# Kernel tuning notes

Hardware: AMD Instinct MI355X
Metric: run time of the kernel (lower is better)

## Reference

```python
import jax, jax.numpy as jnp
import numpy as np

DIM = 512
B, S = 4, 2048


def _linear_params(key, d_in, d_out):
    kw, kb = jax.random.split(key)
    bound = 1.0 / np.sqrt(d_in)
    W = jax.random.uniform(kw, (d_out, d_in), minval=-bound, maxval=bound, dtype=jnp.float32)
    b = jax.random.uniform(kb, (d_out,), minval=-bound, maxval=bound, dtype=jnp.float32)
    return W, b


def setup_inputs() -> dict:
    key = jax.random.key(0)
    ks = jax.random.split(key, 6)
    x = jax.random.normal(ks[0], (B, S, DIM), dtype=jnp.float32)
    Wq, bq = _linear_params(ks[1], DIM, DIM)
    Wk, bk = _linear_params(ks[2], DIM, DIM)
    Wv, bv = _linear_params(ks[3], DIM, DIM)
    W1, b1 = _linear_params(ks[4], DIM, 4 * DIM)
    W2, b2 = _linear_params(ks[5], 4 * DIM, DIM)
    return {"x": x, "Wq": Wq, "bq": bq, "Wk": Wk, "bk": bk,
            "Wv": Wv, "bv": bv, "W1": W1, "b1": b1, "W2": W2, "b2": b2}


def reference(x, Wq, bq, Wk, bk, Wv, bv, W1, b1, W2, b2):
    # q, k, v projections (torch Linear: x @ W.T + b)
    q = x @ Wq.T + bq          # [B, S, D]
    k = x @ Wk.T + bk
    v = x @ Wv.T + bv
    # unscaled attention, exactly as in the source (no 1/sqrt(d))
    scores = jnp.einsum('bsd,btd->bst', q, k)   # [B, S, S]
    attn = jax.nn.softmax(scores, axis=-1) @ v  # [B, S, D]
    # 2-layer FFN with ReLU
    h = jax.nn.relu(attn @ W1.T + b1)           # [B, S, 4D]
    return h @ W2.T + b2                        # [B, S, D]
```

## Files before the change

### kernel.cpp

```cpp
#include <hip/hip_runtime.h>
#include <hip/hip_bf16.h>

typedef _Float16  f16x8  __attribute__((ext_vector_type(8)));
typedef float     f32x4  __attribute__((ext_vector_type(4)));
typedef unsigned short u16;
typedef u16       u16x4  __attribute__((ext_vector_type(4)));
typedef u16       u16x8  __attribute__((ext_vector_type(8)));

#define LOG2E 1.44269504f

__device__ __forceinline__ u16 f2h_bits(float f) {
    union { _Float16 h; u16 u; } v; v.h = (_Float16)f; return v.u;
}
__device__ __forceinline__ float h2f(u16 b) {
    union { u16 u; _Float16 h; } v; v.u = b; return (float)v.h;
}

__global__ __launch_bounds__(256)
void cvt_all(const float* __restrict__ x,
             const float* __restrict__ Wq, const float* __restrict__ Wk,
             const float* __restrict__ Wv, const float* __restrict__ W1,
             const float* __restrict__ W2, const float* __restrict__ bq,
             const float* __restrict__ bk, const float* __restrict__ bv,
             u16* __restrict__ x16, u16* __restrict__ Wqkv16,
             u16* __restrict__ W116, u16* __restrict__ W216, float* __restrict__ bqkv) {
    const int i = blockIdx.x * 256 + threadIdx.x;
    constexpr int X4 = 8192 * 512 / 4;
    constexpr int S = 512 * 512 / 4, L = 2048 * 512 / 4;
    const float* src; u16* dst; int j;
    if      (i < X4)                 { src = x;  dst = x16;            j = i;                  }
    else if (i < X4 + S)             { src = Wq; dst = Wqkv16;         j = i - X4;             }
    else if (i < X4 + 2 * S)         { src = Wk; dst = Wqkv16 + 4 * S; j = i - X4 - S;         }
    else if (i < X4 + 3 * S)         { src = Wv; dst = Wqkv16 + 8 * S; j = i - X4 - 2 * S;     }
    else if (i < X4 + 3 * S + L)     { src = W1; dst = W116;           j = i - X4 - 3 * S;     }
    else if (i < X4 + 3 * S + 2 * L) { src = W2; dst = W216;           j = i - X4 - 3 * S - L; }
    else if (i < X4 + 3 * S + 2 * L + 384) {
        const int g = (i - X4 - 3 * S - 2 * L) * 4;
#pragma unroll
        for (int t = 0; t < 4; ++t) {
            const int e = g + t;
            bqkv[e] = (e < 512) ? bq[e] : (e < 1024 ? bk[e - 512] : bv[e - 1024]);
        }
        return;
    } else return;
    f32x4 v = ((const f32x4*)src)[j];
    u16x4 h;
#pragma unroll
    for (int t = 0; t < 4; ++t) h[t] = f2h_bits(v[t]);
    ((u16x4*)dst)[j] = h;
}

template<int ROWS>
__device__ __forceinline__ void stage_rows(const u16* __restrict__ g0, int ld, u16* lds, int wl) {
    const int l = threadIdx.x & 63;
    constexpr int CH = ROWS / 64;
#pragma unroll
    for (int i = 0; i < CH; ++i) {
        const int base = (wl * CH + i) << 10;
        const int off  = base + (l << 4);
        const int row  = off >> 6;
        const int cb   = off & 63;
        const u16* g = g0 + (size_t)row * ld + (cb >> 1);
        __builtin_amdgcn_global_load_lds((const __attribute__((address_space(1))) void*)g,
                                         (__attribute__((address_space(3))) void*)((char*)lds + base),
                                         16, 0, 0);
    }
}

template<int BN, int SPLITK, bool RELU, int OMODE, bool AEXP, typename TC>
__global__ __launch_bounds__(256 * SPLITK, 4)
void gemm16(const u16* __restrict__ Ag, const u16* __restrict__ Bg,
            const float* __restrict__ bias, TC* __restrict__ C,
            void* __restrict__ xtra, const void* __restrict__ xtra2,
            int K, int lda, int ldb, int ldc,
            long sA, long sB, long sC)
{
    const int nx = gridDim.x, ny = gridDim.y;
    const int nwg = nx * ny * gridDim.z;
    int bid = blockIdx.x + nx * (blockIdx.y + ny * blockIdx.z);
    int swz = (bid & 7) * (nwg >> 3) + (bid >> 3);
    const int n0 = (swz % nx) * BN; swz /= nx;
    const int m0 = (swz % ny) * 128;
    const int bz = swz / ny;

    constexpr int FR = (BN == 128) ? 4 : 2;
    constexpr int ATILE = 128 * 32;
    constexpr int BTILE = BN * 32;
    constexpr int BUFSZ = ATILE + BTILE;
    __shared__ __align__(16) u16 smem[SPLITK * 2 * BUFSZ];

    const int l  = threadIdx.x & 63, w = threadIdx.x >> 6;
    const int kw = (SPLITK == 2) ? (w >> 2) : 0;
    const int wl = w & 3;
    const int wr = (BN == 128) ? (wl >> 1) * 64 : wl * 32;
    const int wc = (BN == 128) ? (wl & 1) * 64 : 0;
    const int lr = l & 15, kg = l >> 4;

    const int Kh = K / SPLITK;
    const int kb = kw * Kh;

    const u16* Ab = Ag + (size_t)bz * sA + (size_t)m0 * lda + kb;
    const u16* Bb = Bg + (size_t)bz * sB + (size_t)n0 * ldb + kb;
    const float* Cb = AEXP ? ((const float*)xtra2 + (size_t)bz * 2048 * 32 + (size_t)m0 * 32)
                           : nullptr;
    C += (size_t)bz * sC;

    u16* mybuf = smem + kw * 2 * BUFSZ;

    u16x8 areg0, areg1; float acof0, acof1;
    auto stage_issue = [&](int buf, int k0) {
        u16* s = mybuf + buf * BUFSZ;
        if constexpr (AEXP) {
            {
                const int off = ((wl * 2 + 0) << 10) + (l << 4);
                const int row = off >> 6, col = (off & 63) >> 1;
                areg0 = *(const u16x8*)&Ab[(size_t)row * lda + k0 + col];
                acof0 = Cb[row * 32 + ((kb + k0) >> 6)];
            }
            {
                const int off = ((wl * 2 + 1) << 10) + (l << 4);
                const int row = off >> 6, col = (off & 63) >> 1;
                areg1 = *(const u16x8*)&Ab[(size_t)row * lda + k0 + col];
                acof1 = Cb[row * 32 + ((kb + k0) >> 6)];
            }
        } else {
            stage_rows<128>(Ab + k0, lda, s, wl);
        }
        stage_rows<BN>(Bb + k0, ldb, s + ATILE, wl);
    };
    auto stage_finish = [&](int buf) {
        if constexpr (AEXP) {
            u16* s = mybuf + buf * BUFSZ;
            {
                const int off = ((wl * 2 + 0) << 10) + (l << 4);
                u16x8 o;
#pragma unroll
                for (int j = 0; j < 8; ++j)
                    o[j] = f2h_bits(exp2f(h2f(areg0[j]) * LOG2E + acof0));
                *(u16x8*)((char*)s + off) = o;
            }
            {
                const int off = ((wl * 2 + 1) << 10) + (l << 4);
                u16x8 o;
#pragma unroll
                for (int j = 0; j < 8; ++j)
                    o[j] = f2h_bits(exp2f(h2f(areg1[j]) * LOG2E + acof1));
                *(u16x8*)((char*)s + off) = o;
            }
        }
    };

    f32x4 acc[FR][4] = {};
    auto compute = [&](int buf) {
        const u16* sA = mybuf + buf * BUFSZ;
        const u16* sB = sA + ATILE;
        f16x8 a[FR], b[4];
#pragma unroll
        for (int i = 0; i < FR; ++i) a[i] = *(const f16x8*)&sA[(wr + i * 16 + lr) * 32 + kg * 8];
#pragma unroll
        for (int i = 0; i < 4; ++i)  b[i] = *(const f16x8*)&sB[(wc + i * 16 + lr) * 32 + kg * 8];
#pragma unroll
        for (int mi = 0; mi < FR; ++mi)
#pragma unroll
            for (int ni = 0; ni < 4; ++ni)
                acc[mi][ni] = __builtin_amdgcn_mfma_f32_16x16x32_f16(a[mi], b[ni], acc[mi][ni], 0, 0, 0);
    };

    stage_issue(0, 0);
    stage_finish(0);
    __syncthreads();
    int cur = 0;
    for (int k0 = 0; k0 < Kh; k0 += 32) {
        const bool more = (k0 + 32 < Kh);
        if (more) stage_issue(cur ^ 1, k0 + 32);
        compute(cur);
        if (more) stage_finish(cur ^ 1);
        __syncthreads();
        cur ^= 1;
    }

    if constexpr (SPLITK == 2) {
        float* red = (float*)smem;
        const int slot = (wl * 64 + l) * (FR * 4);
        if (kw == 1) {
#pragma unroll
            for (int mi = 0; mi < FR; ++mi)
#pragma unroll
                for (int ni = 0; ni < 4; ++ni)
                    *(f32x4*)&red[(slot + mi * 4 + ni) * 4] = acc[mi][ni];
        }
        __syncthreads();
        if (kw == 1) return;
#pragma unroll
        for (int mi = 0; mi < FR; ++mi)
#pragma unroll
            for (int ni = 0; ni < 4; ++ni)
                acc[mi][ni] += *(const f32x4*)&red[(slot + mi * 4 + ni) * 4];
    }

    if constexpr (OMODE == 5) {
        float* MB = (float*)xtra + (size_t)bz * 2048 * 32;
        float* SB = (float*)const_cast<void*>(xtra2);
        SB += (size_t)bz * 2048 * 32;
        const int cb = (n0 + wc) >> 6;
#pragma unroll
        for (int mi = 0; mi < FR; ++mi) {
            const int mbase = m0 + wr + mi * 16 + kg * 4;
#pragma unroll
            for (int j = 0; j < 4; ++j) {
                float rmax = fmaxf(fmaxf(acc[mi][0][j], acc[mi][1][j]),
                                   fmaxf(acc[mi][2][j], acc[mi][3][j]));
                rmax = fmaxf(rmax, __shfl_xor(rmax, 1));
                rmax = fmaxf(rmax, __shfl_xor(rmax, 2));
                rmax = fmaxf(rmax, __shfl_xor(rmax, 4));
                rmax = fmaxf(rmax, __shfl_xor(rmax, 8));
                float lsum = 0.0f;
#pragma unroll
                for (int ni = 0; ni < 4; ++ni) lsum += __expf(acc[mi][ni][j] - rmax);
                lsum += __shfl_xor(lsum, 1);
                lsum += __shfl_xor(lsum, 2);
                lsum += __shfl_xor(lsum, 4);
                lsum += __shfl_xor(lsum, 8);
                const int row = mbase + j;
                if (lr == 0) {
                    MB[(size_t)row * 32 + cb] = rmax;
                    SB[(size_t)row * 32 + cb] = lsum;
                }
#pragma unroll
                for (int ni = 0; ni < 4; ++ni)
                    ((u16*)C)[(size_t)row * ldc + (n0 + wc + ni * 16 + lr)] =
                        f2h_bits(acc[mi][ni][j] - rmax);
            }
        }
        return;
    }

#pragma unroll
    for (int mi = 0; mi < FR; ++mi) {
        const int mbase = m0 + wr + mi * 16 + kg * 4;
#pragma unroll
        for (int ni = 0; ni < 4; ++ni) {
            const int n = n0 + wc + ni * 16 + lr;
            const float bv = bias ? bias[n] : 0.0f;
            if constexpr (OMODE == 4) {
                if (n0 < 1024) {
#pragma unroll
                    for (int j = 0; j < 4; ++j)
                        ((u16*)C)[(size_t)(mbase + j) * ldc + n] = f2h_bits(acc[mi][ni][j] + bv);
                } else {
                    const int d  = n - 1024;
                    const int bb = mbase >> 11;
                    const int s  = mbase & 2047;
                    u16x4 o;
#pragma unroll
                    for (int j = 0; j < 4; ++j) o[j] = f2h_bits(acc[mi][ni][j] + bv);
                    *(u16x4*)((u16*)xtra + ((size_t)bb * 512 + d) * 2048 + s) = o;
                }
            } else {
#pragma unroll
                for (int j = 0; j < 4; ++j) {
                    float x = acc[mi][ni][j] + bv;
                    if constexpr (RELU) x = fmaxf(x, 0.0f);
                    const size_t idx = (size_t)(mbase + j) * ldc + n;
                    if constexpr (OMODE == 0) C[idx] = x;
                    else                      ((u16*)C)[idx] = f2h_bits(x);
                }
            }
        }
    }
}

__global__ __launch_bounds__(256)
void softmax_stats(const float* __restrict__ MB, const float* __restrict__ SB,
                   float* __restrict__ Cc) {
    const int row = blockIdx.x * 256 + threadIdx.x;
    const f32x4* mbp = (const f32x4*)(MB + (size_t)row * 32);
    const f32x4* sbp = (const f32x4*)(SB + (size_t)row * 32);
    f32x4 mv[8], sv[8];
#pragma unroll
    for (int i = 0; i < 8; ++i) { mv[i] = mbp[i]; sv[i] = sbp[i]; }
    float m = mv[0][0];
#pragma unroll
    for (int i = 0; i < 8; ++i)
#pragma unroll
        for (int j = 0; j < 4; ++j) m = fmaxf(m, mv[i][j]);
    float s = 0.0f;
#pragma unroll
    for (int i = 0; i < 8; ++i)
#pragma unroll
        for (int j = 0; j < 4; ++j) s += sv[i][j] * __expf(mv[i][j] - m);
    const float lg = __log2f(s);
    f32x4* cp = (f32x4*)(Cc + (size_t)row * 32);
#pragma unroll
    for (int i = 0; i < 8; ++i) {
        f32x4 o;
#pragma unroll
        for (int j = 0; j < 4; ++j) o[j] = (mv[i][j] - m) * LOG2E - lg;
        cp[i] = o;
    }
}

extern "C" void kernel_launch(void* const* d_in, const int* in_sizes, int n_in,
                              void* d_out, int out_size, void* d_ws, size_t ws_size,
                              hipStream_t stream) {
    const float* x  = (const float*)d_in[0];
    const float* Wq = (const float*)d_in[1];
    const float* bq = (const float*)d_in[2];
    const float* Wk = (const float*)d_in[3];
    const float* bk = (const float*)d_in[4];
    const float* Wv = (const float*)d_in[5];
    const float* bv = (const float*)d_in[6];
    const float* W1 = (const float*)d_in[7];
    const float* b1 = (const float*)d_in[8];
    const float* W2 = (const float*)d_in[9];
    const float* b2 = (const float*)d_in[10];
    float* out = (float*)d_out;

    char* ws = (char*)d_ws;
    size_t off = 0;
    auto alloc = [&](size_t bytes) { void* p = ws + off; off += (bytes + 255) & ~(size_t)255; return p; };
    u16* x16    = (u16*)alloc(8192ull * 512 * 2);
    u16* Wqkv16 = (u16*)alloc(1536ull * 512 * 2);
    u16* W116   = (u16*)alloc(2048ull * 512 * 2);
    u16* W216   = (u16*)alloc(512ull * 2048 * 2);
    float* bqkv = (float*)alloc(1536 * 4);
    u16* qk     = (u16*)alloc(8192ull * 1024 * 2);
    u16* s16    = (u16*)alloc(4ull * 2048 * 2048 * 2);
    u16* vt     = (u16*)alloc(4ull * 512 * 2048 * 2);
    float* mb   = (float*)alloc(8192ull * 32 * 4);
    float* sb   = (float*)alloc(8192ull * 32 * 4);
    float* cf   = (float*)alloc(8192ull * 32 * 4);
    u16* attn = x16;
    u16* h    = s16;
    if (ws_size < off) return;

    dim3 blk(256), blk2(512);

    cvt_all<<<dim3(6914), blk, 0, stream>>>(x, Wq, Wk, Wv, W1, W2, bq, bk, bv,
                                            x16, Wqkv16, W116, W216, bqkv);

    gemm16<128, 1, false, 4, false, u16><<<dim3(12, 64, 1), blk, 0, stream>>>(
        x16, Wqkv16, bqkv, qk, vt, nullptr, 512, 512, 512, 1024, 0, 0, 0);
    gemm16<128, 1, false, 5, false, u16><<<dim3(16, 16, 4), blk, 0, stream>>>(
        qk, qk + 512, nullptr, s16, mb, sb, 512, 1024, 1024, 2048,
        2048L * 1024, 2048L * 1024, 2048L * 2048);
    softmax_stats<<<dim3(32), blk, 0, stream>>>(mb, sb, cf);
    gemm16<64, 2, false, 2, true, u16><<<dim3(8, 16, 4), blk2, 0, stream>>>(
        s16, vt, nullptr, attn, nullptr, cf, 2048, 2048, 2048, 512,
        2048L * 2048, 512L * 2048, 2048L * 512);
    gemm16<128, 1, true, 2, false, u16><<<dim3(16, 64, 1), blk, 0, stream>>>(
        attn, W116, b1, h, nullptr, nullptr, 512, 512, 512, 2048, 0, 0, 0);
    gemm16<64, 2, false, 0, false, float><<<dim3(8, 64, 1), blk2, 0, stream>>>(
        h, W216, b2, out, nullptr, nullptr, 2048, 2048, 2048, 512, 0, 0, 0);
}
```

Measured before the change: 199.4 us.

## Store block-local softmax probabilities and rescale PV partials per column block

The QK^T kernel now writes exp(s - local block max) as fp16 instead of the raw shifted scores. The PV GEMM loads A through the async global-to-LDS path instead of doing exp in registers, keeping per-64-column partial accumulators and folding them into the output with a per-row scale factor computed by softmax_stats. This removes the per-element exp from the PV GEMM's A-staging path, at the cost of extra accumulator registers and a scaled accumulate every two k-steps.

Result: faster. 183.1 us (-8.2%).

```diff
diff --git a/kernel.cpp b/kernel.cpp
--- a/kernel.cpp
+++ b/kernel.cpp
@@ -7,13 +7,8 @@
 typedef u16       u16x4  __attribute__((ext_vector_type(4)));
 typedef u16       u16x8  __attribute__((ext_vector_type(8)));
 
-#define LOG2E 1.44269504f
-
 __device__ __forceinline__ u16 f2h_bits(float f) {
     union { _Float16 h; u16 u; } v; v.h = (_Float16)f; return v.u;
-}
-__device__ __forceinline__ float h2f(u16 b) {
-    union { u16 u; _Float16 h; } v; v.u = b; return (float)v.h;
 }
 
 __global__ __launch_bounds__(256)
@@ -67,7 +62,7 @@
     }
 }
 
-template<int BN, int SPLITK, bool RELU, int OMODE, bool AEXP, typename TC>
+template<int BN, int SPLITK, bool RELU, int OMODE, bool PVS, typename TC>
 __global__ __launch_bounds__(256 * SPLITK, 4)
 void gemm16(const u16* __restrict__ Ag, const u16* __restrict__ Bg,
             const float* __restrict__ bias, TC* __restrict__ C,
@@ -101,56 +96,19 @@
 
     const u16* Ab = Ag + (size_t)bz * sA + (size_t)m0 * lda + kb;
     const u16* Bb = Bg + (size_t)bz * sB + (size_t)n0 * ldb + kb;
-    const float* Cb = AEXP ? ((const float*)xtra2 + (size_t)bz * 2048 * 32 + (size_t)m0 * 32)
-                           : nullptr;
+    const float* Cb = PVS ? ((const float*)xtra2 + (size_t)bz * 2048 * 32) : nullptr;
     C += (size_t)bz * sC;
 
     u16* mybuf = smem + kw * 2 * BUFSZ;
 
-    u16x8 areg0, areg1; float acof0, acof1;
-    auto stage_issue = [&](int buf, int k0) {
+    auto stage = [&](int buf, int k0) {
         u16* s = mybuf + buf * BUFSZ;
-        if constexpr (AEXP) {
-            {
-                const int off = ((wl * 2 + 0) << 10) + (l << 4);
-                const int row = off >> 6, col = (off & 63) >> 1;
-                areg0 = *(const u16x8*)&Ab[(size_t)row * lda + k0 + col];
-                acof0 = Cb[row * 32 + ((kb + k0) >> 6)];
-            }
-            {
-                const int off = ((wl * 2 + 1) << 10) + (l << 4);
-                const int row = off >> 6, col = (off & 63) >> 1;
-                areg1 = *(const u16x8*)&Ab[(size_t)row * lda + k0 + col];
-                acof1 = Cb[row * 32 + ((kb + k0) >> 6)];
-            }
-        } else {
-            stage_rows<128>(Ab + k0, lda, s, wl);
-        }
+        stage_rows<128>(Ab + k0, lda, s, wl);
         stage_rows<BN>(Bb + k0, ldb, s + ATILE, wl);
     };
-    auto stage_finish = [&](int buf) {
-        if constexpr (AEXP) {
-            u16* s = mybuf + buf * BUFSZ;
-            {
-                const int off = ((wl * 2 + 0) << 10) + (l << 4);
-                u16x8 o;
-#pragma unroll
-                for (int j = 0; j < 8; ++j)
-                    o[j] = f2h_bits(exp2f(h2f(areg0[j]) * LOG2E + acof0));
-                *(u16x8*)((char*)s + off) = o;
-            }
-            {
-                const int off = ((wl * 2 + 1) << 10) + (l << 4);
-                u16x8 o;
-#pragma unroll
-                for (int j = 0; j < 8; ++j)
-                    o[j] = f2h_bits(exp2f(h2f(areg1[j]) * LOG2E + acof1));
-                *(u16x8*)((char*)s + off) = o;
-            }
-        }
-    };
 
     f32x4 acc[FR][4] = {};
+    f32x4 tmp[FR][4] = {};
     auto compute = [&](int buf) {
         const u16* sA = mybuf + buf * BUFSZ;
         const u16* sB = sA + ATILE;
@@ -162,19 +120,38 @@
 #pragma unroll
         for (int mi = 0; mi < FR; ++mi)
 #pragma unroll
-            for (int ni = 0; ni < 4; ++ni)
-                acc[mi][ni] = __builtin_amdgcn_mfma_f32_16x16x32_f16(a[mi], b[ni], acc[mi][ni], 0, 0, 0);
+            for (int ni = 0; ni < 4; ++ni) {
+                if constexpr (PVS)
+                    tmp[mi][ni] = __builtin_amdgcn_mfma_f32_16x16x32_f16(a[mi], b[ni], tmp[mi][ni], 0, 0, 0);
+                else
+                    acc[mi][ni] = __builtin_amdgcn_mfma_f32_16x16x32_f16(a[mi], b[ni], acc[mi][ni], 0, 0, 0);
+            }
     };
 
-    stage_issue(0, 0);
-    stage_finish(0);
+    stage(0, 0);
     __syncthreads();
     int cur = 0;
     for (int k0 = 0; k0 < Kh; k0 += 32) {
-        const bool more = (k0 + 32 < Kh);
-        if (more) stage_issue(cur ^ 1, k0 + 32);
+        if (k0 + 32 < Kh) stage(cur ^ 1, k0 + 32);
         compute(cur);
-        if (more) stage_finish(cur ^ 1);
+        if constexpr (PVS) {
+            if (k0 & 32) {
+                const int cb = (kb + k0) >> 6;
+#pragma unroll
+                for (int mi = 0; mi < FR; ++mi) {
+                    const int mrow = m0 + wr + mi * 16 + kg * 4;
+                    f32x4 cf4;
+#pragma unroll
+                    for (int j = 0; j < 4; ++j) cf4[j] = Cb[(size_t)(mrow + j) * 32 + cb];
+#pragma unroll
+                    for (int ni = 0; ni < 4; ++ni) {
+#pragma unroll
+                        for (int j = 0; j < 4; ++j) acc[mi][ni][j] += cf4[j] * tmp[mi][ni][j];
+                        tmp[mi][ni] = f32x4{0.f, 0.f, 0.f, 0.f};
+                    }
+                }
+            }
+        }
         __syncthreads();
         cur ^= 1;
     }
@@ -214,9 +191,9 @@
                 rmax = fmaxf(rmax, __shfl_xor(rmax, 2));
                 rmax = fmaxf(rmax, __shfl_xor(rmax, 4));
                 rmax = fmaxf(rmax, __shfl_xor(rmax, 8));
-                float lsum = 0.0f;
-#pragma unroll
-                for (int ni = 0; ni < 4; ++ni) lsum += __expf(acc[mi][ni][j] - rmax);
+                float p[4]; float lsum = 0.0f;
+#pragma unroll
+                for (int ni = 0; ni < 4; ++ni) { p[ni] = __expf(acc[mi][ni][j] - rmax); lsum += p[ni]; }
                 lsum += __shfl_xor(lsum, 1);
                 lsum += __shfl_xor(lsum, 2);
                 lsum += __shfl_xor(lsum, 4);
@@ -228,8 +205,7 @@
                 }
 #pragma unroll
                 for (int ni = 0; ni < 4; ++ni)
-                    ((u16*)C)[(size_t)row * ldc + (n0 + wc + ni * 16 + lr)] =
-                        f2h_bits(acc[mi][ni][j] - rmax);
+                    ((u16*)C)[(size_t)row * ldc + (n0 + wc + ni * 16 + lr)] = f2h_bits(p[ni]);
             }
         }
         return;
@@ -272,7 +248,7 @@
 
 __global__ __launch_bounds__(256)
 void softmax_stats(const float* __restrict__ MB, const float* __restrict__ SB,
-                   float* __restrict__ Cc) {
+                   float* __restrict__ Cf) {
     const int row = blockIdx.x * 256 + threadIdx.x;
     const f32x4* mbp = (const f32x4*)(MB + (size_t)row * 32);
     const f32x4* sbp = (const f32x4*)(SB + (size_t)row * 32);
@@ -284,18 +260,18 @@
     for (int i = 0; i < 8; ++i)
 #pragma unroll
         for (int j = 0; j < 4; ++j) m = fmaxf(m, mv[i][j]);
-    float s = 0.0f;
+    float e[8][4]; float s = 0.0f;
 #pragma unroll
     for (int i = 0; i < 8; ++i)
 #pragma unroll
-        for (int j = 0; j < 4; ++j) s += sv[i][j] * __expf(mv[i][j] - m);
-    const float lg = __log2f(s);
-    f32x4* cp = (f32x4*)(Cc + (size_t)row * 32);
+        for (int j = 0; j < 4; ++j) { e[i][j] = __expf(mv[i][j] - m); s += sv[i][j] * e[i][j]; }
+    const float inv = 1.0f / s;
+    f32x4* cp = (f32x4*)(Cf + (size_t)row * 32);
 #pragma unroll
     for (int i = 0; i < 8; ++i) {
         f32x4 o;
 #pragma unroll
-        for (int j = 0; j < 4; ++j) o[j] = (mv[i][j] - m) * LOG2E - lg;
+        for (int j = 0; j < 4; ++j) o[j] = e[i][j] * inv;
         cp[i] = o;
     }
 }
@@ -325,13 +301,13 @@
     u16* W216   = (u16*)alloc(512ull * 2048 * 2);
     float* bqkv = (float*)alloc(1536 * 4);
     u16* qk     = (u16*)alloc(8192ull * 1024 * 2);
-    u16* s16    = (u16*)alloc(4ull * 2048 * 2048 * 2);
+    u16* p16    = (u16*)alloc(4ull * 2048 * 2048 * 2);
     u16* vt     = (u16*)alloc(4ull * 512 * 2048 * 2);
     float* mb   = (float*)alloc(8192ull * 32 * 4);
     float* sb   = (float*)alloc(8192ull * 32 * 4);
     float* cf   = (float*)alloc(8192ull * 32 * 4);
     u16* attn = x16;
-    u16* h    = s16;
+    u16* h    = p16;
     if (ws_size < off) return;
 
     dim3 blk(256), blk2(512);
@@ -342,11 +318,11 @@
     gemm16<128, 1, false, 4, false, u16><<<dim3(12, 64, 1), blk, 0, stream>>>(
         x16, Wqkv16, bqkv, qk, vt, nullptr, 512, 512, 512, 1024, 0, 0, 0);
     gemm16<128, 1, false, 5, false, u16><<<dim3(16, 16, 4), blk, 0, stream>>>(
-        qk, qk + 512, nullptr, s16, mb, sb, 512, 1024, 1024, 2048,
+        qk, qk + 512, nullptr, p16, mb, sb, 512, 1024, 1024, 2048,
         2048L * 1024, 2048L * 1024, 2048L * 2048);
     softmax_stats<<<dim3(32), blk, 0, stream>>>(mb, sb, cf);
     gemm16<64, 2, false, 2, true, u16><<<dim3(8, 16, 4), blk2, 0, stream>>>(
-        s16, vt, nullptr, attn, nullptr, cf, 2048, 2048, 2048, 512,
+        p16, vt, nullptr, attn, nullptr, cf, 2048, 2048, 2048, 512,
         2048L * 2048, 512L * 2048, 2048L * 512);
     gemm16<128, 1, true, 2, false, u16><<<dim3(16, 64, 1), blk, 0, stream>>>(
         attn, W116, b1, h, nullptr, nullptr, 512, 512, 512, 2048, 0, 0, 0);
```
